# Kernel optimization log

Measured on AMD Instinct MI355X. Metric: run time of the kernel, lower is better.

## Reference

```python
import jax, jax.numpy as jnp
import numpy as np

N, E, IN, H, OUT, G = 100000, 1600000, 9, 64, 6, 1024
EPS = 1e-5


def setup_inputs() -> dict:
    key = jax.random.key(0)
    ks = jax.random.split(key, 24)
    inp = {
        "x": jax.random.normal(ks[0], (N, IN), dtype=jnp.float32),
        "edge_index": jax.random.randint(ks[1], (2, E), 0, N, dtype=jnp.int64),
        "edge_weight": jax.random.uniform(ks[2], (E,), dtype=jnp.float32),
        "batch": jnp.sort(jax.random.randint(ks[3], (N,), 0, G, dtype=jnp.int64)),
    }
    def lin(k, fan_in, fan_out):
        return jax.random.normal(k, (fan_in, fan_out), dtype=jnp.float32) / np.sqrt(fan_in)
    # GraphConv layer 0: IN -> H; layers 1,2: H -> H
    inp["W_rel0"], inp["W_root0"], inp["b0"] = lin(ks[4], IN, H), lin(ks[5], IN, H), jnp.zeros((H,), jnp.float32)
    inp["W_rel1"], inp["W_root1"], inp["b1"] = lin(ks[6], H, H), lin(ks[7], H, H), jnp.zeros((H,), jnp.float32)
    inp["W_rel2"], inp["W_root2"], inp["b2"] = lin(ks[8], H, H), lin(ks[9], H, H), jnp.zeros((H,), jnp.float32)
    # BatchNorm params for the first num_layers-1 = 2 layers
    inp["g0"], inp["be0"] = jnp.ones((H,), jnp.float32), jnp.zeros((H,), jnp.float32)
    inp["g1"], inp["be1"] = jnp.ones((H,), jnp.float32), jnp.zeros((H,), jnp.float32)
    # MLP head
    inp["W_l1"], inp["b_l1"] = lin(ks[10], H, H), jnp.zeros((H,), jnp.float32)
    inp["W_l2"], inp["b_l2"] = lin(ks[11], H, OUT), jnp.zeros((OUT,), jnp.float32)
    return inp


def graph_conv(x, src, dst, ew, W_rel, W_root, b):
    # PyG GraphConv: out = aggr_add(e_ji * x_j) @ W_rel + b + x @ W_root
    msg = x[src] * ew[:, None]                      # [E, F] gather
    agg = jax.ops.segment_sum(msg, dst, num_segments=x.shape[0])  # [N, F] scatter-add
    return agg @ W_rel + b + x @ W_root


def batch_norm(x, g, b):
    m = jnp.mean(x, axis=0)
    v = jnp.var(x, axis=0)
    return (x - m) * jax.lax.rsqrt(v + EPS) * g + b


def reference(x, edge_index, edge_weight, batch,
              W_rel0, W_root0, b0, W_rel1, W_root1, b1, W_rel2, W_root2, b2,
              g0, be0, g1, be1, W_l1, b_l1, W_l2, b_l2):
    src, dst = edge_index[0], edge_index[1]
    # layer 0: conv -> BN -> relu (dropout p applied only in training; eval here)
    h = graph_conv(x, src, dst, edge_weight, W_rel0, W_root0, b0)
    h = jax.nn.relu(batch_norm(h, g0, be0))
    # layer 1
    h = graph_conv(h, src, dst, edge_weight, W_rel1, W_root1, b1)
    h = jax.nn.relu(batch_norm(h, g1, be1))
    # layer 2 (no norm/relu)
    h = graph_conv(h, src, dst, edge_weight, W_rel2, W_root2, b2)
    # global mean pool over graphs
    summed = jax.ops.segment_sum(h, batch, num_segments=G)            # [G, H]
    counts = jax.ops.segment_sum(jnp.ones((h.shape[0],), h.dtype), batch, num_segments=G)
    pooled = summed / jnp.maximum(counts, 1.0)[:, None]
    # MLP head
    z = jax.nn.relu(pooled @ W_l1 + b_l1)
    return z @ W_l2 + b_l2
```

## Files before the change

### kernel.cpp

```cpp
#include <hip/hip_runtime.h>
#include <hip/hip_fp16.h>

constexpr int N    = 100000;
constexpr int E    = 1600000;
constexpr int FIN  = 9;
constexpr int OUTF = 6;
constexpr int G    = 1024;
constexpr int NPB  = 256;
constexpr int NB   = (N + NPB - 1) / NPB;
constexpr int CH   = 2048;
constexpr int NCH  = (E + CH - 1) / CH;
constexpr int BCAP = 4864;
constexpr int CBCAP= BCAP + NPB + 8;
constexpr int EBUF = 5888;
constexpr int ZCNT = 256 + G * 64;

typedef _Float16 f16x8 __attribute__((ext_vector_type(8)));
typedef float    f32x4 __attribute__((ext_vector_type(4)));

__device__ __forceinline__ void atomAddF(float* p, float v) { unsafeAtomicAdd(p, v); }

__global__ __launch_bounds__(256) void initK(int* __restrict__ cursor, float* __restrict__ zeros)
{
    int i = blockIdx.x * 256 + threadIdx.x;
    if (i < NB) cursor[i] = i * BCAP;
    if (i < ZCNT) zeros[i] = 0.f;
}

__global__ __launch_bounds__(256) void passA(const int* __restrict__ src, const int* __restrict__ dst,
    const float* __restrict__ ew, int* __restrict__ cursor, int2* __restrict__ bucketed)
{
    __shared__ int h[NB];
    __shared__ int hb[NB];
    int t = threadIdx.x;
    for (int i = t; i < NB; i += 256) h[i] = 0;
    __syncthreads();
    int base = blockIdx.x * CH;
    int myS[8], myD[8], rk[8]; float myW[8];
#pragma unroll
    for (int i = 0; i < 8; i++) {
        int e = base + i * 256 + t;
        if (e < E) {
            myS[i] = src[e]; myD[i] = dst[e]; myW[i] = ew[e];
            rk[i] = atomicAdd(&h[myD[i] >> 8], 1);
        } else myD[i] = -1;
    }
    __syncthreads();
    for (int i = t; i < NB; i += 256) hb[i] = h[i] ? atomicAdd(&cursor[i], h[i]) : 0;
    __syncthreads();
#pragma unroll
    for (int i = 0; i < 8; i++) if (myD[i] >= 0) {
        int packed = myS[i] | ((myD[i] & 255) << 24);
        bucketed[hb[myD[i] >> 8] + rk[i]] = make_int2(packed, __float_as_int(myW[i]));
    }
}

__global__ __launch_bounds__(NPB) void passB(const int* __restrict__ cursor,
    const int2* __restrict__ bucketed, int* __restrict__ ebeg, int* __restrict__ eend,
    int2* __restrict__ csr)
{
    __shared__ int2 ebuf[EBUF];
    __shared__ int cl[NPB], sa[NPB], sb[NPB], curs[NPB];
    int b = blockIdx.x, t = threadIdx.x;
    int node0 = b * NPB;
    int nnode = min(NPB, N - node0);
    int cnt = cursor[b] - b * BCAP;
    int abase = b * BCAP;
    int base = b * CBCAP;
    bool fits = (cnt <= EBUF);
    cl[t] = 0;
    __syncthreads();
    for (int e = t; e < cnt; e += NPB) {
        int2 r = bucketed[abase + e];
        if (fits) ebuf[e] = r;
        atomicAdd(&cl[((unsigned)r.x) >> 24], 1);
    }
    __syncthreads();
    int deg = cl[t];
    int pc = (deg + 1) & ~1;
    int* cur = sa; int* nxt = sb;
    cur[t] = pc;
    __syncthreads();
    for (int o = 1; o < NPB; o <<= 1) {
        int v = cur[t];
        if (t >= o) v += cur[t - o];
        nxt[t] = v;
        __syncthreads();
        int* tmp = cur; cur = nxt; nxt = tmp;
    }
    int off = cur[t] - pc;
    if (t < nnode) { ebeg[node0 + t] = base + off; eend[node0 + t] = base + off + deg; }
    curs[t] = off;
    __syncthreads();
    for (int e = t; e < cnt; e += NPB) {
        int2 r = fits ? ebuf[e] : bucketed[abase + e];
        int dl = ((unsigned)r.x) >> 24;
        int pos = base + atomicAdd(&curs[dl], 1);
        csr[pos] = make_int2(r.x & 0x00FFFFFF, r.y);
    }
    __syncthreads();
    if (t < nnode && (deg & 1)) csr[base + off + deg] = make_int2(0, 0);
    if (t < 4) csr[base + cur[NPB - 1] + t] = make_int2(0, 0);
}

__global__ __launch_bounds__(256) void proj0(const float* __restrict__ Ain,
    const float* __restrict__ Wrel, const float* __restrict__ Wroot,
    const float* __restrict__ bias, __half* __restrict__ P, __half* __restrict__ Hout)
{
    int t = threadIdx.x, j = t & 63;
    int nl = __builtin_amdgcn_readfirstlane(t >> 6);
    float wrel[FIN], wroot[FIN];
#pragma unroll
    for (int k = 0; k < FIN; k++) { wrel[k] = Wrel[k * 64 + j]; wroot[k] = Wroot[k * 64 + j]; }
    float bj = bias[j];
    const int ntiles = N / 4;
    for (int tile = blockIdx.x; tile < ntiles; tile += gridDim.x) {
        int n = tile * 4 + nl;
        const float* r = Ain + (size_t)n * FIN;
        float ap = 0.f, ar = bj;
#pragma unroll
        for (int k = 0; k < FIN; k++) {
            float h = r[k];
            ap = fmaf(h, wrel[k], ap);
            ar = fmaf(h, wroot[k], ar);
        }
        P[(size_t)n * 64 + j]    = __float2half(ap);
        Hout[(size_t)n * 64 + j] = __float2half(ar);
    }
}

__global__ __launch_bounds__(256) void wprep(const float* __restrict__ Wrel1, const float* __restrict__ Wroot1,
    const float* __restrict__ Wrel2, const float* __restrict__ Wroot2, __half* __restrict__ Wt)
{
    int i = blockIdx.x * 256 + threadIdx.x;
    int layer = i >> 13, r = i & 8191;
    int c = r >> 6, k = r & 63;
    const float* Wrel = layer ? Wrel2 : Wrel1;
    const float* Wroot = layer ? Wroot2 : Wroot1;
    float v = (c < 64) ? Wrel[k * 64 + c] : Wroot[k * 64 + (c - 64)];
    Wt[i] = __float2half(v);
}

__global__ __launch_bounds__(256) void projm(const __half* __restrict__ Hin, const __half* __restrict__ Wt,
    const float* __restrict__ bias, __half* __restrict__ P, __half* __restrict__ Hout)
{
    int t = threadIdx.x, lane = t & 63;
    int wv = blockIdx.x * 4 + (t >> 6);
    int nw = gridDim.x * 4;
    int n16 = lane & 15, quad = lane >> 4;
    f16x8 bf[8][2];
#pragma unroll
    for (int ct = 0; ct < 8; ct++)
#pragma unroll
        for (int kh = 0; kh < 2; kh++)
            bf[ct][kh] = *(const f16x8*)(Wt + (size_t)(ct * 16 + n16) * 64 + kh * 32 + quad * 8);
    float bcol[4];
#pragma unroll
    for (int i = 0; i < 4; i++) bcol[i] = bias[i * 16 + n16];
    const int NT = N / 16;
    for (int tile = wv; tile < NT; tile += nw) {
        int n0 = tile * 16;
        f16x8 a0 = *(const f16x8*)(Hin + (size_t)(n0 + n16) * 64 + quad * 8);
        f16x8 a1 = *(const f16x8*)(Hin + (size_t)(n0 + n16) * 64 + 32 + quad * 8);
        f32x4 acc[8];
#pragma unroll
        for (int ct = 0; ct < 8; ct++) {
            f32x4 c = {0.f, 0.f, 0.f, 0.f};
            c = __builtin_amdgcn_mfma_f32_16x16x32_f16(a0, bf[ct][0], c, 0, 0, 0);
            c = __builtin_amdgcn_mfma_f32_16x16x32_f16(a1, bf[ct][1], c, 0, 0, 0);
            acc[ct] = c;
        }
#pragma unroll
        for (int ct = 0; ct < 8; ct++) {
#pragma unroll
            for (int r = 0; r < 4; r++) {
                int n = n0 + quad * 4 + r;
                if (ct < 4) P[(size_t)n * 64 + ct * 16 + n16] = __float2half(acc[ct][r]);
                else Hout[(size_t)n * 64 + (ct - 4) * 16 + n16] = __float2half(acc[ct][r] + bcol[ct - 4]);
            }
        }
    }
}

template<int EPI>
__global__ __launch_bounds__(256) void gather(const __half* __restrict__ P, __half* H,
    const int2* __restrict__ csr, const int* __restrict__ ebeg, const int* __restrict__ eend,
    float* __restrict__ stats, const int* __restrict__ batch, float* __restrict__ pool)
{
    int t = threadIdx.x, lane = t & 63;
    int wv = (blockIdx.x * blockDim.x + t) >> 6;
    int nw = (gridDim.x * blockDim.x) >> 6;
    float s1 = 0.f, s2 = 0.f;
    const int NPAIR = N / 2;
    for (int pr = wv; pr < NPAIR; pr += nw) {
        int n0 = 2 * pr, n1 = n0 + 1;
        int b0 = ebeg[n0], m0 = (eend[n0] - b0 + 1) >> 1;
        int b1 = ebeg[n1], m1 = (eend[n1] - b1 + 1) >> 1;
        const int4* q0 = (const int4*)csr + (b0 >> 1);
        const int4* q1 = (const int4*)csr + (b1 >> 1);
        int c0 = max(m0 - 1, 0), c1 = max(m1 - 1, 0);
        float x0 = __half2float(H[(size_t)n0 * 64 + lane]);
        float x1 = __half2float(H[(size_t)n1 * 64 + lane]);
        float a0 = 0.f, a1 = 0.f, a2 = 0.f, a3 = 0.f;
        float a4 = 0.f, a5 = 0.f, a6 = 0.f, a7 = 0.f;
        int mm = max(m0, m1);
        for (int k = 0; k < mm; k += 2) {
            int4 qa = q0[min(k,     c0)];
            int4 qb = q0[min(k + 1, c0)];
            int4 qc = q1[min(k,     c1)];
            int4 qd = q1[min(k + 1, c1)];
            float pa0 = __half2float(P[(size_t)qa.x * 64 + lane]);
            float pa1 = __half2float(P[(size_t)qa.z * 64 + lane]);
            float pb0 = __half2float(P[(size_t)qb.x * 64 + lane]);
            float pb1 = __half2float(P[(size_t)qb.z * 64 + lane]);
            float pc0 = __half2float(P[(size_t)qc.x * 64 + lane]);
            float pc1 = __half2float(P[(size_t)qc.z * 64 + lane]);
            float pd0 = __half2float(P[(size_t)qd.x * 64 + lane]);
            float pd1 = __half2float(P[(size_t)qd.z * 64 + lane]);
            float wa = (k     < m0) ? __int_as_float(qa.y) : 0.f;
            float wA = (k     < m0) ? __int_as_float(qa.w) : 0.f;
            float wb = (k + 1 < m0) ? __int_as_float(qb.y) : 0.f;
            float wB = (k + 1 < m0) ? __int_as_float(qb.w) : 0.f;
            float wc = (k     < m1) ? __int_as_float(qc.y) : 0.f;
            float wC = (k     < m1) ? __int_as_float(qc.w) : 0.f;
            float wd = (k + 1 < m1) ? __int_as_float(qd.y) : 0.f;
            float wD = (k + 1 < m1) ? __int_as_float(qd.w) : 0.f;
            a0 = fmaf(wa, pa0, a0); a1 = fmaf(wA, pa1, a1);
            a2 = fmaf(wb, pb0, a2); a3 = fmaf(wB, pb1, a3);
            a4 = fmaf(wc, pc0, a4); a5 = fmaf(wC, pc1, a5);
            a6 = fmaf(wd, pd0, a6); a7 = fmaf(wD, pd1, a7);
        }
        float r0 = x0 + ((a0 + a1) + (a2 + a3));
        float r1 = x1 + ((a4 + a5) + (a6 + a7));
        if constexpr (EPI == 0) {
            H[(size_t)n0 * 64 + lane] = __float2half(r0);
            H[(size_t)n1 * 64 + lane] = __float2half(r1);
            s1 += r0 + r1; s2 += r0 * r0 + r1 * r1;
        } else {
            atomAddF(&pool[batch[n0] * 64 + lane], r0);
            atomAddF(&pool[batch[n1] * 64 + lane], r1);
        }
    }
    if constexpr (EPI == 0) {
        __shared__ float sred[256];
        sred[t] = s1; __syncthreads();
        if (t < 64) atomAddF(&stats[t], sred[t] + sred[t+64] + sred[t+128] + sred[t+192]);
        __syncthreads();
        sred[t] = s2; __syncthreads();
        if (t < 64) atomAddF(&stats[64 + t], sred[t] + sred[t+64] + sred[t+128] + sred[t+192]);
    }
}

__global__ __launch_bounds__(256) void bn_relu(uint4* __restrict__ H4,
    const float* __restrict__ stats, const float* __restrict__ gam, const float* __restrict__ bet)
{
    int i = blockIdx.x * blockDim.x + threadIdx.x;
    constexpr float invN = 1.0f / (float)N;
    int j0 = (i & 7) * 8;
    uint4 v = H4[i];
    unsigned arr[4] = {v.x, v.y, v.z, v.w};
#pragma unroll
    for (int c = 0; c < 4; c++) {
        float2 f = __half22float2(*(const __half2*)&arr[c]);
        int j = j0 + 2 * c;
        float m0 = stats[j] * invN,     vv0 = stats[64 + j] * invN - m0 * m0;
        float m1 = stats[j + 1] * invN, vv1 = stats[64 + j + 1] * invN - m1 * m1;
        float sc0 = gam[j] * rsqrtf(vv0 + 1e-5f),     sh0 = bet[j] - m0 * sc0;
        float sc1 = gam[j + 1] * rsqrtf(vv1 + 1e-5f), sh1 = bet[j + 1] - m1 * sc1;
        f.x = fmaxf(fmaf(f.x, sc0, sh0), 0.f);
        f.y = fmaxf(fmaf(f.y, sc1, sh1), 0.f);
        __half2 h = __float22half2_rn(f);
        arr[c] = *(const unsigned*)&h;
    }
    H4[i] = make_uint4(arr[0], arr[1], arr[2], arr[3]);
}

__global__ __launch_bounds__(64) void head(const float* __restrict__ pool,
    const int* __restrict__ batch, const float* __restrict__ Wl1, const float* __restrict__ bl1,
    const float* __restrict__ Wl2, const float* __restrict__ bl2, float* __restrict__ out)
{
    int g = blockIdx.x, t = threadIdx.x;
    __shared__ float sp[64];
    __shared__ float sz[64];
    __shared__ int scnt;
    if (t == 0) {
        int lo = 0, hi = N;
        while (lo < hi) { int m = (lo + hi) >> 1; if (batch[m] < g) lo = m + 1; else hi = m; }
        int lo2 = lo, hi2 = N;
        while (lo2 < hi2) { int m = (lo2 + hi2) >> 1; if (batch[m] < g + 1) lo2 = m + 1; else hi2 = m; }
        scnt = lo2 - lo;
    }
    __syncthreads();
    float cnt = fmaxf((float)scnt, 1.0f);
    sp[t] = pool[g * 64 + t] / cnt;
    __syncthreads();
    float acc = bl1[t];
#pragma unroll
    for (int k = 0; k < 64; k++) acc = fmaf(sp[k], Wl1[k * 64 + t], acc);
    sz[t] = fmaxf(acc, 0.f);
    __syncthreads();
    if (t < OUTF) {
        float o = bl2[t];
#pragma unroll
        for (int k = 0; k < 64; k++) o = fmaf(sz[k], Wl2[k * OUTF + t], o);
        out[g * OUTF + t] = o;
    }
}

extern "C" void kernel_launch(void* const* d_in, const int* in_sizes, int n_in,
                              void* d_out, int out_size, void* d_ws, size_t ws_size,
                              hipStream_t stream)
{
    const float* x     = (const float*)d_in[0];
    const int*   ei    = (const int*)d_in[1];
    const float* ew    = (const float*)d_in[2];
    const int*   batch = (const int*)d_in[3];
    const float* Wrel0 = (const float*)d_in[4];
    const float* Wroot0= (const float*)d_in[5];
    const float* b0    = (const float*)d_in[6];
    const float* Wrel1 = (const float*)d_in[7];
    const float* Wroot1= (const float*)d_in[8];
    const float* b1    = (const float*)d_in[9];
    const float* Wrel2 = (const float*)d_in[10];
    const float* Wroot2= (const float*)d_in[11];
    const float* b2    = (const float*)d_in[12];
    const float* g0    = (const float*)d_in[13];
    const float* be0   = (const float*)d_in[14];
    const float* g1    = (const float*)d_in[15];
    const float* be1   = (const float*)d_in[16];
    const float* Wl1   = (const float*)d_in[17];
    const float* bl1   = (const float*)d_in[18];
    const float* Wl2   = (const float*)d_in[19];
    const float* bl2   = (const float*)d_in[20];
    const int* srcI = ei;
    const int* dstI = ei + E;

    __half* Ha     = (__half*)d_ws;
    __half* Hb     = Ha + (size_t)N * 64;
    __half* P      = Hb + (size_t)N * 64;
    int2*   csr    = (int2*)(P + (size_t)N * 64);
    int*    ebeg   = (int*)(csr + (size_t)NB * CBCAP);
    int*    eend   = ebeg + N;
    int*    cursor = eend + N;
    float*  stats0 = (float*)(cursor + NB);
    float*  stats1 = stats0 + 128;
    float*  pool   = stats1 + 128;
    __half* Wt1    = (__half*)(pool + G * 64);
    __half* Wt2    = Wt1 + 128 * 64;
    int2*   bucketed = (int2*)Hb;

    initK<<<(ZCNT + 255) / 256, 256, 0, stream>>>(cursor, stats0);
    passA<<<NCH, 256, 0, stream>>>(srcI, dstI, ew, cursor, bucketed);
    passB<<<NB, NPB, 0, stream>>>(cursor, bucketed, ebeg, eend, csr);
    wprep<<<64, 256, 0, stream>>>(Wrel1, Wroot1, Wrel2, Wroot2, Wt1);

    proj0<<<2048, 256, 0, stream>>>(x, Wrel0, Wroot0, b0, P, Ha);
    gather<0><<<2048, 256, 0, stream>>>(P, Ha, csr, ebeg, eend, stats0, nullptr, nullptr);
    bn_relu<<<N * 8 / 256, 256, 0, stream>>>((uint4*)Ha, stats0, g0, be0);

    projm<<<1024, 256, 0, stream>>>(Ha, Wt1, b1, P, Hb);
    gather<0><<<2048, 256, 0, stream>>>(P, Hb, csr, ebeg, eend, stats1, nullptr, nullptr);
    bn_relu<<<N * 8 / 256, 256, 0, stream>>>((uint4*)Hb, stats1, g1, be1);

    projm<<<1024, 256, 0, stream>>>(Hb, Wt2, b2, P, Ha);
    gather<1><<<2048, 256, 0, stream>>>(P, Ha, csr, ebeg, eend, nullptr, batch, pool);

    head<<<G, 64, 0, stream>>>(pool, batch, Wl1, bl1, Wl2, bl2, (float*)d_out);
}
```

Measured before the change: 524.3 us.

## Aggregate raw 9-wide inputs for layer 0 and fuse BN+ReLU into projections

Layer 0 now aggregates the 9-feature fp16 copy of x over edges before projecting, rather than projecting to 64 features first and gathering 64-wide rows. A new post-projection kernel applies both weight matrices, writes H0 and accumulates the BN statistics. The separate bn_relu passes are removed and their normalisation plus ReLU is applied when projm loads each activation tile. This cuts the layer-0 gather traffic and two full read/write passes over the activations, but adds an agg9 buffer and an fp16 conversion of x in initK, and moves the bucketed scratch buffer onto Ha.

```diff
diff --git a/kernel.cpp b/kernel.cpp
--- a/kernel.cpp
+++ b/kernel.cpp
@@ -20,11 +20,13 @@
 
 __device__ __forceinline__ void atomAddF(float* p, float v) { unsafeAtomicAdd(p, v); }
 
-__global__ __launch_bounds__(256) void initK(int* __restrict__ cursor, float* __restrict__ zeros)
+__global__ __launch_bounds__(256) void initK(int* __restrict__ cursor, float* __restrict__ zeros,
+    const float* __restrict__ x, __half* __restrict__ x9)
 {
     int i = blockIdx.x * 256 + threadIdx.x;
     if (i < NB) cursor[i] = i * BCAP;
     if (i < ZCNT) zeros[i] = 0.f;
+    if (i < N * FIN) x9[i] = __float2half(x[i]);
 }
 
 __global__ __launch_bounds__(256) void passA(const int* __restrict__ src, const int* __restrict__ dst,
@@ -103,32 +105,6 @@
     if (t < 4) csr[base + cur[NPB - 1] + t] = make_int2(0, 0);
 }
 
-__global__ __launch_bounds__(256) void proj0(const float* __restrict__ Ain,
-    const float* __restrict__ Wrel, const float* __restrict__ Wroot,
-    const float* __restrict__ bias, __half* __restrict__ P, __half* __restrict__ Hout)
-{
-    int t = threadIdx.x, j = t & 63;
-    int nl = __builtin_amdgcn_readfirstlane(t >> 6);
-    float wrel[FIN], wroot[FIN];
-#pragma unroll
-    for (int k = 0; k < FIN; k++) { wrel[k] = Wrel[k * 64 + j]; wroot[k] = Wroot[k * 64 + j]; }
-    float bj = bias[j];
-    const int ntiles = N / 4;
-    for (int tile = blockIdx.x; tile < ntiles; tile += gridDim.x) {
-        int n = tile * 4 + nl;
-        const float* r = Ain + (size_t)n * FIN;
-        float ap = 0.f, ar = bj;
-#pragma unroll
-        for (int k = 0; k < FIN; k++) {
-            float h = r[k];
-            ap = fmaf(h, wrel[k], ap);
-            ar = fmaf(h, wroot[k], ar);
-        }
-        P[(size_t)n * 64 + j]    = __float2half(ap);
-        Hout[(size_t)n * 64 + j] = __float2half(ar);
-    }
-}
-
 __global__ __launch_bounds__(256) void wprep(const float* __restrict__ Wrel1, const float* __restrict__ Wroot1,
     const float* __restrict__ Wrel2, const float* __restrict__ Wroot2, __half* __restrict__ Wt)
 {
@@ -141,13 +117,89 @@
     Wt[i] = __float2half(v);
 }
 
+__global__ __launch_bounds__(256) void gather9(const __half* __restrict__ x9,
+    const int2* __restrict__ csr, const int* __restrict__ ebeg, const int* __restrict__ eend,
+    float* __restrict__ agg9)
+{
+    int t = threadIdx.x, lane = t & 63;
+    int es = lane >> 4, fc = min(lane & 15, FIN - 1);
+    int wv = (blockIdx.x * blockDim.x + t) >> 6;
+    int nw = (gridDim.x * blockDim.x) >> 6;
+    for (int n = wv; n < N; n += nw) {
+        int beg = ebeg[n], end = eend[n];
+        float a0 = 0.f, a1 = 0.f;
+        for (int k = beg; k < end; k += 8) {
+            int i0 = min(k + es, end - 1);
+            int i1 = min(k + 4 + es, end - 1);
+            int2 eA = csr[i0];
+            int2 eB = csr[i1];
+            float pA = __half2float(x9[(size_t)eA.x * FIN + fc]);
+            float pB = __half2float(x9[(size_t)eB.x * FIN + fc]);
+            float wA = (k + es     < end) ? __int_as_float(eA.y) : 0.f;
+            float wB = (k + 4 + es < end) ? __int_as_float(eB.y) : 0.f;
+            a0 = fmaf(wA, pA, a0);
+            a1 = fmaf(wB, pB, a1);
+        }
+        float r = a0 + a1;
+        r += __shfl(r, lane ^ 16, 64);
+        r += __shfl(r, lane ^ 32, 64);
+        if (lane < FIN) agg9[(size_t)n * FIN + lane] = r;
+    }
+}
+
+__global__ __launch_bounds__(256) void proj0post(const float* __restrict__ x,
+    const float* __restrict__ agg9, const float* __restrict__ Wrel,
+    const float* __restrict__ Wroot, const float* __restrict__ bias,
+    __half* __restrict__ H0, float* __restrict__ stats)
+{
+    int t = threadIdx.x, j = t & 63;
+    int nl = __builtin_amdgcn_readfirstlane(t >> 6);
+    float wrel[FIN], wroot[FIN];
+#pragma unroll
+    for (int k = 0; k < FIN; k++) { wrel[k] = Wrel[k * 64 + j]; wroot[k] = Wroot[k * 64 + j]; }
+    float bj = bias[j];
+    float s1 = 0.f, s2 = 0.f;
+    const int ntiles = N / 4;
+    for (int tile = blockIdx.x; tile < ntiles; tile += gridDim.x) {
+        int n = tile * 4 + nl;
+        const float* xr = x + (size_t)n * FIN;
+        const float* ar = agg9 + (size_t)n * FIN;
+        float acc = bj;
+#pragma unroll
+        for (int k = 0; k < FIN; k++) {
+            acc = fmaf(ar[k], wrel[k], acc);
+            acc = fmaf(xr[k], wroot[k], acc);
+        }
+        H0[(size_t)n * 64 + j] = __float2half(acc);
+        s1 += acc; s2 += acc * acc;
+    }
+    __shared__ float sred[256];
+    sred[t] = s1; __syncthreads();
+    if (t < 64) atomAddF(&stats[t], sred[t] + sred[t+64] + sred[t+128] + sred[t+192]);
+    __syncthreads();
+    sred[t] = s2; __syncthreads();
+    if (t < 64) atomAddF(&stats[64 + t], sred[t] + sred[t+64] + sred[t+128] + sred[t+192]);
+}
+
 __global__ __launch_bounds__(256) void projm(const __half* __restrict__ Hin, const __half* __restrict__ Wt,
-    const float* __restrict__ bias, __half* __restrict__ P, __half* __restrict__ Hout)
+    const float* __restrict__ bias, const float* __restrict__ stats,
+    const float* __restrict__ gam, const float* __restrict__ bet,
+    __half* __restrict__ P, __half* __restrict__ Hout)
 {
     int t = threadIdx.x, lane = t & 63;
     int wv = blockIdx.x * 4 + (t >> 6);
     int nw = gridDim.x * 4;
     int n16 = lane & 15, quad = lane >> 4;
+    constexpr float invN = 1.0f / (float)N;
+    float sc[16], sh[16];
+#pragma unroll
+    for (int jj = 0; jj < 16; jj++) {
+        int k = (jj < 8) ? (quad * 8 + jj) : (32 + quad * 8 + (jj - 8));
+        float m = stats[k] * invN;
+        float v = stats[64 + k] * invN - m * m;
+        sc[jj] = gam[k] * rsqrtf(v + 1e-5f);
+        sh[jj] = bet[k] - m * sc[jj];
+    }
     f16x8 bf[8][2];
 #pragma unroll
     for (int ct = 0; ct < 8; ct++)
@@ -160,8 +212,14 @@
     const int NT = N / 16;
     for (int tile = wv; tile < NT; tile += nw) {
         int n0 = tile * 16;
-        f16x8 a0 = *(const f16x8*)(Hin + (size_t)(n0 + n16) * 64 + quad * 8);
-        f16x8 a1 = *(const f16x8*)(Hin + (size_t)(n0 + n16) * 64 + 32 + quad * 8);
+        f16x8 r0 = *(const f16x8*)(Hin + (size_t)(n0 + n16) * 64 + quad * 8);
+        f16x8 r1 = *(const f16x8*)(Hin + (size_t)(n0 + n16) * 64 + 32 + quad * 8);
+        f16x8 a0, a1;
+#pragma unroll
+        for (int jj = 0; jj < 8; jj++) {
+            a0[jj] = (_Float16)fmaxf(fmaf((float)r0[jj], sc[jj],     sh[jj]),     0.f);
+            a1[jj] = (_Float16)fmaxf(fmaf((float)r1[jj], sc[jj + 8], sh[jj + 8]), 0.f);
+        }
         f32x4 acc[8];
 #pragma unroll
         for (int ct = 0; ct < 8; ct++) {
@@ -251,30 +309,6 @@
     }
 }
 
-__global__ __launch_bounds__(256) void bn_relu(uint4* __restrict__ H4,
-    const float* __restrict__ stats, const float* __restrict__ gam, const float* __restrict__ bet)
-{
-    int i = blockIdx.x * blockDim.x + threadIdx.x;
-    constexpr float invN = 1.0f / (float)N;
-    int j0 = (i & 7) * 8;
-    uint4 v = H4[i];
-    unsigned arr[4] = {v.x, v.y, v.z, v.w};
-#pragma unroll
-    for (int c = 0; c < 4; c++) {
-        float2 f = __half22float2(*(const __half2*)&arr[c]);
-        int j = j0 + 2 * c;
-        float m0 = stats[j] * invN,     vv0 = stats[64 + j] * invN - m0 * m0;
-        float m1 = stats[j + 1] * invN, vv1 = stats[64 + j + 1] * invN - m1 * m1;
-        float sc0 = gam[j] * rsqrtf(vv0 + 1e-5f),     sh0 = bet[j] - m0 * sc0;
-        float sc1 = gam[j + 1] * rsqrtf(vv1 + 1e-5f), sh1 = bet[j + 1] - m1 * sc1;
-        f.x = fmaxf(fmaf(f.x, sc0, sh0), 0.f);
-        f.y = fmaxf(fmaf(f.y, sc1, sh1), 0.f);
-        __half2 h = __float22half2_rn(f);
-        arr[c] = *(const unsigned*)&h;
-    }
-    H4[i] = make_uint4(arr[0], arr[1], arr[2], arr[3]);
-}
-
 __global__ __launch_bounds__(64) void head(const float* __restrict__ pool,
     const int* __restrict__ batch, const float* __restrict__ Wl1, const float* __restrict__ bl1,
     const float* __restrict__ Wl2, const float* __restrict__ bl2, float* __restrict__ out)
@@ -347,22 +381,22 @@
     float*  pool   = stats1 + 128;
     __half* Wt1    = (__half*)(pool + G * 64);
     __half* Wt2    = Wt1 + 128 * 64;
-    int2*   bucketed = (int2*)Hb;
-
-    initK<<<(ZCNT + 255) / 256, 256, 0, stream>>>(cursor, stats0);
+    float*  agg9   = (float*)(Wt2 + 128 * 64);
+    __half* x9     = (__half*)(agg9 + (size_t)N * FIN);
+    int2*   bucketed = (int2*)Ha;
+
+    initK<<<(N * FIN + 255) / 256, 256, 0, stream>>>(cursor, stats0, x, x9);
     passA<<<NCH, 256, 0, stream>>>(srcI, dstI, ew, cursor, bucketed);
     passB<<<NB, NPB, 0, stream>>>(cursor, bucketed, ebeg, eend, csr);
     wprep<<<64, 256, 0, stream>>>(Wrel1, Wroot1, Wrel2, Wroot2, Wt1);
 
-    proj0<<<2048, 256, 0, stream>>>(x, Wrel0, Wroot0, b0, P, Ha);
-    gather<0><<<2048, 256, 0, stream>>>(P, Ha, csr, ebeg, eend, stats0, nullptr, nullptr);
-    bn_relu<<<N * 8 / 256, 256, 0, stream>>>((uint4*)Ha, stats0, g0, be0);
-
-    projm<<<1024, 256, 0, stream>>>(Ha, Wt1, b1, P, Hb);
+    gather9<<<2048, 256, 0, stream>>>(x9, csr, ebeg, eend, agg9);
+    proj0post<<<2048, 256, 0, stream>>>(x, agg9, Wrel0, Wroot0, b0, Ha, stats0);
+
+    projm<<<1024, 256, 0, stream>>>(Ha, Wt1, b1, stats0, g0, be0, P, Hb);
     gather<0><<<2048, 256, 0, stream>>>(P, Hb, csr, ebeg, eend, stats1, nullptr, nullptr);
-    bn_relu<<<N * 8 / 256, 256, 0, stream>>>((uint4*)Hb, stats1, g1, be1);
-
-    projm<<<1024, 256, 0, stream>>>(Hb, Wt2, b2, P, Ha);
+
+    projm<<<1024, 256, 0, stream>>>(Hb, Wt2, b2, stats1, g1, be1, P, Ha);
     gather<1><<<2048, 256, 0, stream>>>(P, Ha, csr, ebeg, eend, nullptr, batch, pool);
 
     head<<<G, 64, 0, stream>>>(pool, batch, Wl1, bl1, Wl2, bl2, (float*)d_out);
```

After: 490.1 us. -6.5%, faster.
